# Performance work log

Measured on AMD Instinct MI355X. Metric: run time of the kernel, lower is better.

Reference implementation:

```python
import jax, jax.numpy as jnp
import numpy as np

EMBED_DIM = 584  # module-global, used as softmax scale base (C ** -0.5)


def setup_inputs() -> dict:
    key = jax.random.key(0)
    ks = jax.random.split(key, 7)
    B, T, C, H, D = 16, 1024, 584, 8, 73
    x = jax.random.normal(ks[0], (B, T, C), dtype=jnp.float32)
    memory = jax.random.normal(ks[1], (B, T, C), dtype=jnp.float32)
    s = 0.02
    Wq = jax.random.normal(ks[2], (H, C, D), dtype=jnp.float32) * s
    Wk = jax.random.normal(ks[3], (H, C, D), dtype=jnp.float32) * s
    Wv = jax.random.normal(ks[4], (H, C, D), dtype=jnp.float32) * s
    Wp = jax.random.normal(ks[5], (C, C), dtype=jnp.float32) * s
    bp = jnp.zeros((C,), dtype=jnp.float32)
    return {"x": x, "memory": memory, "Wq": Wq, "Wk": Wk, "Wv": Wv, "Wp": Wp, "bp": bp}


def reference(x, memory, Wq, Wk, Wv, Wp, bp):
    B, T, C = x.shape
    # per-head projections, vectorized over heads: [B, H, T, D]
    q = jnp.einsum('btc,hcd->bhtd', x, Wq)
    k = jnp.einsum('bsc,hcd->bhsd', memory, Wk)
    v = jnp.einsum('btc,hcd->bhtd', x, Wv)  # NOTE: value from x, per original code
    # scale uses full embed dim C (not head size), per original code
    scores = jnp.einsum('bhtd,bhsd->bhts', q, k) * (C ** -0.5)
    weights = jax.nn.softmax(scores, axis=-1)
    # dropout is identity in eval/reference mode
    out = jnp.einsum('bhts,bhsd->bhtd', weights, v)  # requires S == T (matches original)
    out = out.transpose(0, 2, 1, 3).reshape(B, T, C)  # concat heads on last dim
    out = out @ Wp + bp  # output projection (dropout identity)
    return out
```

## Files before the change

### kernel.cpp

```cpp
#include <hip/hip_runtime.h>
#include <hip/hip_bf16.h>

typedef unsigned short u16;
typedef __attribute__((ext_vector_type(4))) unsigned short u16x4;
typedef __attribute__((ext_vector_type(8))) unsigned short u16x8;
typedef __attribute__((ext_vector_type(8))) __bf16 bf16x8;
typedef __attribute__((ext_vector_type(4))) float f32x4;

#define BB 16
#define TSEQ 1024
#define CC 584
#define HH 8
#define DHD 73
#define NR (BB*TSEQ)
#define KPW 640
#define DP 96
#define HD (HH*DP)
#define NP3 768
#define PPITCH 88
#define CEXP 0.0596985934f

__device__ __forceinline__ u16 f2bf(float f) {
  __bf16 h = (__bf16)f;
  return __builtin_bit_cast(u16, h);
}
__device__ __forceinline__ bf16x8 as_bf(u16x8 v) { return __builtin_bit_cast(bf16x8, v); }

#define GLL16(g, l) __builtin_amdgcn_global_load_lds( \
    (const __attribute__((address_space(1))) void*)(g), \
    (__attribute__((address_space(3))) void*)(l), 16, 0, 0)

#define BARRIER() asm volatile("s_barrier" ::: "memory")
#define LGKM0()   asm volatile("s_waitcnt lgkmcnt(0)" ::: "memory")
#define VMW8()    asm volatile("s_waitcnt vmcnt(8)" ::: "memory")
#define VMW4()    asm volatile("s_waitcnt vmcnt(4)" ::: "memory")
#define VMW0()    asm volatile("s_waitcnt vmcnt(0)" ::: "memory")

#define PKA 10240
#define PKB2 720
#define PKC2 240
__global__ void pack_all_kernel(const float* __restrict__ x, const float* __restrict__ mem,
                                const float* __restrict__ Wq, const float* __restrict__ Wk,
                                const float* __restrict__ Wv, const float* __restrict__ Wp,
                                u16* __restrict__ xmb, u16* __restrict__ wt,
                                u16* __restrict__ wpt) {
  const int bidx = blockIdx.x;
  const int tid = threadIdx.x;
  if (bidx < PKA) {
    int idx = bidx * 256 + tid;
    int row = idx / (KPW / 8);
    int c8  = (idx % (KPW / 8)) * 8;
    u16x8 o = {0, 0, 0, 0, 0, 0, 0, 0};
    if (c8 < CC) {
      const float* src = (row < NR) ? &x[(size_t)row * CC + c8]
                                    : &mem[(size_t)(row - NR) * CC + c8];
      f32x4 a = *(const f32x4*)src;
      f32x4 b = *(const f32x4*)(src + 4);
#pragma unroll
      for (int t = 0; t < 4; t++) { o[t] = f2bf(a[t]); o[4 + t] = f2bf(b[t]); }
    }
    *(u16x8*)&xmb[(size_t)row * KPW + c8] = o;
  } else if (bidx < PKA + PKB2) {
    const int base = (bidx - PKA) * 2048 + tid;
#pragma unroll
    for (int e = 0; e < 8; e++) {
      int idx = base + e * 256;
      int w   = idx / (HD * KPW);
      int rem = idx % (HD * KPW);
      int n = rem / KPW;
      int k = rem % KPW;
      int h = n / DP, d = n % DP;
      u16 val = 0;
      if (d < DHD && k < CC) {
        const float* W = (w == 0) ? Wq : ((w == 1) ? Wv : Wk);
        val = f2bf(W[((size_t)h * CC + k) * DHD + d]);
      }
      wt[idx] = val;
    }
  } else {
    const int base = (bidx - PKA - PKB2) * 2048 + tid;
#pragma unroll
    for (int e = 0; e < 8; e++) {
      int idx = base + e * 256;
      int n = idx / KPW;
      int c = idx % KPW;
      u16 val = 0;
      if (n < CC && c < CC) val = f2bf(Wp[(size_t)c * CC + n]);
      wpt[idx] = val;
    }
  }
}


template <int BUF, int MH>
__device__ __forceinline__ void rd_a(bf16x8 (&a)[4][2], const u16* lds, int arow,
                                     int sw0, int sw1) {
#pragma unroll
  for (int mq = 0; mq < 4; mq++) {
    const int r = BUF * 32768 + MH * 8192 + arow + mq * 1024;
    a[mq][0] = as_bf(*(const u16x8*)&lds[r + sw0]);
    a[mq][1] = as_bf(*(const u16x8*)&lds[r + sw1]);
  }
}
template <int BUF, int NH>
__device__ __forceinline__ void rd_b(bf16x8 (&b)[2][2], const u16* lds, int brow,
                                     int sw0, int sw1) {
#pragma unroll
  for (int nq = 0; nq < 2; nq++) {
    const int r = BUF * 32768 + 16384 + NH * 8192 + brow + nq * 1024;
    b[nq][0] = as_bf(*(const u16x8*)&lds[r + sw0]);
    b[nq][1] = as_bf(*(const u16x8*)&lds[r + sw1]);
  }
}
template <int BUF, int RG>
__device__ __forceinline__ void stg(const u16* gA, const u16* gB, u16* ldst, int t) {
  const u16* src = (RG < 2) ? gA : gB;
  const int rrow = (RG & 1) * 128;
  const int loff = BUF * 32768 + (RG >> 1) * 16384 + (RG & 1) * 8192;
  GLL16(src + (size_t)rrow * KPW + (size_t)t * 64, ldst + loff);
  GLL16(src + (size_t)(rrow + 64) * KPW + (size_t)t * 64, ldst + loff + 4096);
}
template <int MH, int NH>
__device__ __forceinline__ void mmq(f32x4 (&acc)[8][4], const bf16x8 (&a)[4][2],
                                    const bf16x8 (&b)[2][2]) {
  __builtin_amdgcn_s_setprio(1);
#pragma unroll
  for (int mq = 0; mq < 4; mq++)
#pragma unroll
    for (int nq = 0; nq < 2; nq++) {
      f32x4 c = acc[MH * 4 + mq][NH * 2 + nq];
      c = __builtin_amdgcn_mfma_f32_16x16x32_bf16(a[mq][0], b[nq][0], c, 0, 0, 0);
      c = __builtin_amdgcn_mfma_f32_16x16x32_bf16(a[mq][1], b[nq][1], c, 0, 0, 0);
      acc[MH * 4 + mq][NH * 2 + nq] = c;
    }
  __builtin_amdgcn_s_setprio(0);
}

template <int MODE>
__global__ __launch_bounds__(512, 2) void gemm8_kernel(
    const u16* __restrict__ A, const u16* __restrict__ Bt,
    void* __restrict__ CoutV, void* __restrict__ CoutV2,
    const float* __restrict__ bias) {
  extern __shared__ u16 lds[];
  const int tid  = threadIdx.x;
  const int lane = tid & 63;
  const int q15  = lane & 15;
  const int quad = lane >> 4;
  const int wave = tid >> 6;
  const int wmi  = wave >> 2;
  const int wni  = wave & 3;

  const int cpx = gridDim.x >> 3;
  const int bid = (blockIdx.x & 7) * cpx + (blockIdx.x >> 3);

  int m0, n0, npart;
  if (MODE == 4) {
    if (bid < 384) {
      m0 = (bid / 6) * 256; int nt = bid % 6;
      n0 = nt * 256; npart = (nt >= 3) ? 1 : 0;
    } else {
      int b2 = bid - 384;
      m0 = NR + (b2 / 3) * 256; n0 = 1536 + (b2 % 3) * 256; npart = 2;
    }
  } else {
    m0 = (bid / 3) * 256; n0 = (bid % 3) * 256; npart = 0;
  }

  const int tr   = tid >> 3;
  const int scol = ((tid & 7) ^ (tr & 7)) * 8;
  const u16* gA = &A[(size_t)(m0 + tr) * KPW + scol];
  const u16* gB = &Bt[(size_t)(n0 + tr) * KPW + scol];
  u16* ldst = &lds[tid * 8];

  const int rb  = q15 & 7;
  const int sw0 = (quad ^ rb) * 8;
  const int sw1 = ((quad + 4) ^ rb) * 8;
  const int arow = (wmi * 64 + q15) * 64;
  const int brow = (wni * 32 + q15) * 64;

  f32x4 acc[8][4];
#pragma unroll
  for (int i = 0; i < 8; i++)
#pragma unroll
    for (int j = 0; j < 4; j++) acc[i][j] = (f32x4){0.f, 0.f, 0.f, 0.f};
  bf16x8 a[4][2], b0[2][2], b1[2][2];

  stg<0, 0>(gA, gB, ldst, 0);
  stg<0, 2>(gA, gB, ldst, 0);
  stg<0, 3>(gA, gB, ldst, 0);
  stg<0, 1>(gA, gB, ldst, 0);
  stg<1, 0>(gA, gB, ldst, 1);
  stg<1, 2>(gA, gB, ldst, 1);
  VMW8(); BARRIER();

#pragma unroll 1
  for (int i = 0; i < 5; ++i) {
    const int t1 = 2 * i + 1;
    const int t2 = 2 * i + 2;
    const int t3 = 2 * i + 3;
    const bool st = (i < 4);
    rd_a<0, 0>(a, lds, arow, sw0, sw1);
    rd_b<0, 0>(b0, lds, brow, sw0, sw1);
    stg<1, 3>(gA, gB, ldst, t1);
    stg<1, 1>(gA, gB, ldst, t1);
    VMW8(); BARRIER(); LGKM0();
    mmq<0, 0>(acc, a, b0);
    BARRIER();
    rd_b<0, 1>(b1, lds, brow, sw0, sw1);
    BARRIER(); LGKM0();
    mmq<0, 1>(acc, a, b1);
    BARRIER();
    rd_a<0, 1>(a, lds, arow, sw0, sw1);
    BARRIER(); LGKM0();
    mmq<1, 0>(acc, a, b0);
    BARRIER();
    if (st) { stg<0, 0>(gA, gB, ldst, t2); stg<0, 2>(gA, gB, ldst, t2); VMW8(); }
    else { VMW4(); }
    BARRIER();
    mmq<1, 1>(acc, a, b1);
    BARRIER();
    rd_a<1, 0>(a, lds, arow, sw0, sw1);
    rd_b<1, 0>(b0, lds, brow, sw0, sw1);
    if (st) { stg<0, 3>(gA, gB, ldst, t2); stg<0, 1>(gA, gB, ldst, t2); VMW8(); }
    else { VMW0(); }
    BARRIER(); LGKM0();
    mmq<0, 0>(acc, a, b0);
    BARRIER();
    rd_b<1, 1>(b1, lds, brow, sw0, sw1);
    BARRIER(); LGKM0();
    mmq<0, 1>(acc, a, b1);
    BARRIER();
    rd_a<1, 1>(a, lds, arow, sw0, sw1);
    BARRIER(); LGKM0();
    mmq<1, 0>(acc, a, b0);
    BARRIER();
    if (st) { stg<1, 0>(gA, gB, ldst, t3); stg<1, 2>(gA, gB, ldst, t3); VMW8(); }
    BARRIER();
    mmq<1, 1>(acc, a, b1);
    BARRIER();
  }

  const int rowb = m0 + wmi * 64 + quad * 4;
  const int colb = n0 + wni * 32 + q15;
#pragma unroll
  for (int mh = 0; mh < 2; mh++)
#pragma unroll
    for (int mq = 0; mq < 4; mq++)
#pragma unroll
      for (int nh = 0; nh < 2; nh++)
#pragma unroll
        for (int nq = 0; nq < 2; nq++) {
          const f32x4 av = acc[mh * 4 + mq][nh * 2 + nq];
          const int row = rowb + mh * 128 + mq * 16;
          const int col = colb + nh * 128 + nq * 16;
          if (MODE == 4) {
            if (npart == 2) {
              u16* Cout = (u16*)CoutV2;
              const int rk = row - NR;
              const int ck = col - 1536;
#pragma unroll
              for (int r = 0; r < 4; r++)
                Cout[(size_t)(rk + r) * HD + ck] = f2bf(av[r]);
            } else if (npart == 0) {
              u16* Cout = (u16*)CoutV;
#pragma unroll
              for (int r = 0; r < 4; r++)
                Cout[(size_t)(row + r) * HD + col] = f2bf(av[r]);
            } else {
              u16* Cout = (u16*)CoutV;
              const int vn = col - HD;
              const int bb = row >> 10;
              const int tl = row & 1023;
              u16x4 pk;
#pragma unroll
              for (int r = 0; r < 4; r++) pk[r] = f2bf(av[r]);
              *(u16x4*)&Cout[(size_t)(NR * HD) + ((size_t)(bb * HD + vn)) * TSEQ + tl] = pk;
            }
          } else {
            if (col < CC) {
              float* Cout = (float*)CoutV;
              const float bvv = bias[col];
#pragma unroll
              for (int r = 0; r < 4; r++)
                Cout[(size_t)(row + r) * CC + col] = av[r] + bvv;
            }
          }
        }
}

__global__ __launch_bounds__(256, 3) void attn_kernel(
    const u16* __restrict__ qb, const u16* __restrict__ kb,
    const u16* __restrict__ vt, u16* __restrict__ attn) {
  __shared__ u16 smem[128 * 96 + 64 * 104 + 96 * 72];
  u16* Qs = smem;
  u16* Ks = smem + 128 * 96;
  u16* Vs = smem + 128 * 96 + 64 * 104;
  u16* Pt = smem;

  const int tid  = threadIdx.x;
  const int lane = tid & 63;
  const int wave = tid >> 6;
  const int q15  = lane & 15;
  const int quad = lane >> 4;
  const int bid  = blockIdx.x;
  const int loc  = bid >> 3;
  const int pair = (bid & 7) * 16 + (loc >> 3);
  const int b  = pair >> 3;
  const int h  = pair & 7;
  const int t0 = (loc & 7) * 128;
  const int wq0 = wave * 32;

  int krow[3], kc[3], vrow[3], vc[3];
#pragma unroll
  for (int p = 0; p < 3; p++) {
    int qk = tid + 256 * p;
    krow[p] = qk / 12; kc[p] = (qk % 12) * 8;
    int qv = tid + 256 * p;
    vrow[p] = qv / 8;  vc[p] = (qv % 8) * 8;
  }
  const u16* kbase = &kb[(size_t)(b * TSEQ) * HD + h * DP];
  const u16* vbase = &vt[(size_t)(b * HD + h * DP) * TSEQ];

  for (int q = tid; q < 128 * 12; q += 256) {
    int row = q / 12, c8 = (q % 12) * 8;
    *(u16x8*)&Qs[row * 96 + c8] =
        *(const u16x8*)&qb[(size_t)(b * TSEQ + t0 + row) * HD + h * DP + c8];
  }
  if (tid < 128) {
    const u16x8 z = {0, 0, 0, 0, 0, 0, 0, 0};
    size_t base = (size_t)(b * TSEQ + t0 + tid) * KPW + CC;
#pragma unroll
    for (int c = 0; c < (KPW - CC) / 8; c++) *(u16x8*)&attn[base + c * 8] = z;
  }
  __syncthreads();

  bf16x8 aq[2][3];
#pragma unroll
  for (int n = 0; n < 2; n++)
#pragma unroll
    for (int kcx = 0; kcx < 3; kcx++)
      aq[n][kcx] = as_bf(*(const u16x8*)&Qs[(wq0 + n * 16 + q15) * 96 + kcx * 32 + quad * 8]);

  float lsum[2] = {0.f, 0.f};
  f32x4 oacc[2][6];
#pragma unroll
  for (int m = 0; m < 2; m++)
#pragma unroll
    for (int jd = 0; jd < 6; jd++) oacc[m][jd] = (f32x4){0.f, 0.f, 0.f, 0.f};

  u16* Ptw = &Pt[wave * 32 * PPITCH];

  u16x8 kreg[3], vreg[3];
#pragma unroll
  for (int p = 0; p < 3; p++) {
    kreg[p] = *(const u16x8*)&kbase[(size_t)krow[p] * HD + kc[p]];
    vreg[p] = *(const u16x8*)&vbase[(size_t)vrow[p] * TSEQ + vc[p]];
  }

  for (int si = 0; si < 16; ++si) {
#pragma unroll
    for (int p = 0; p < 3; p++) {
      *(u16x8*)&Ks[krow[p] * 104 + kc[p]] = kreg[p];
      *(u16x8*)&Vs[vrow[p] * 72 + vc[p]]  = vreg[p];
    }
    __syncthreads();

    if (si < 15) {
      const int s1 = (si + 1) * 64;
#pragma unroll
      for (int p = 0; p < 3; p++) {
        kreg[p] = *(const u16x8*)&kbase[(size_t)(s1 + krow[p]) * HD + kc[p]];
        vreg[p] = *(const u16x8*)&vbase[(size_t)vrow[p] * TSEQ + s1 + vc[p]];
      }
    }

    f32x4 st[4][2];
#pragma unroll
    for (int mt = 0; mt < 4; mt++)
#pragma unroll
      for (int n = 0; n < 2; n++) st[mt][n] = (f32x4){0.f, 0.f, 0.f, 0.f};
    __builtin_amdgcn_s_setprio(1);
#pragma unroll
    for (int kcx = 0; kcx < 3; kcx++) {
      bf16x8 ak[4];
#pragma unroll
      for (int mt = 0; mt < 4; mt++)
        ak[mt] = as_bf(*(const u16x8*)&Ks[(mt * 16 + q15) * 104 + kcx * 32 + quad * 8]);
#pragma unroll
      for (int mt = 0; mt < 4; mt++)
#pragma unroll
        for (int n = 0; n < 2; n++)
          st[mt][n] = __builtin_amdgcn_mfma_f32_16x16x32_bf16(ak[mt], aq[n][kcx], st[mt][n], 0, 0, 0);
    }
    __builtin_amdgcn_s_setprio(0);

#pragma unroll
    for (int mt = 0; mt < 4; mt++)
#pragma unroll
      for (int n = 0; n < 2; n++) {
        f32x4 pv;
#pragma unroll
        for (int r = 0; r < 4; r++) pv[r] = __builtin_amdgcn_exp2f(st[mt][n][r] * CEXP);
        lsum[n] += (pv[0] + pv[1]) + (pv[2] + pv[3]);
        u16x4 pk;
#pragma unroll
        for (int r = 0; r < 4; r++) pk[r] = f2bf(pv[r]);
        *(u16x4*)&Ptw[(n * 16 + q15) * PPITCH + mt * 16 + quad * 4] = pk;
      }

    __builtin_amdgcn_s_setprio(1);
#pragma unroll
    for (int kcx = 0; kcx < 2; kcx++) {
      bf16x8 ap[2];
#pragma unroll
      for (int m = 0; m < 2; m++)
        ap[m] = as_bf(*(const u16x8*)&Ptw[(m * 16 + q15) * PPITCH + kcx * 32 + quad * 8]);
#pragma unroll
      for (int jd = 0; jd < 6; jd++) {
        bf16x8 bv = as_bf(*(const u16x8*)&Vs[(jd * 16 + q15) * 72 + kcx * 32 + quad * 8]);
#pragma unroll
        for (int m = 0; m < 2; m++)
          oacc[m][jd] = __builtin_amdgcn_mfma_f32_16x16x32_bf16(ap[m], bv, oacc[m][jd], 0, 0, 0);
      }
    }
    __builtin_amdgcn_s_setprio(0);
    __syncthreads();
  }

  float lr[2];
#pragma unroll
  for (int n = 0; n < 2; n++) {
    float s = lsum[n];
    s += __shfl_xor(s, 16);
    s += __shfl_xor(s, 32);
    lr[n] = s;
  }

#pragma unroll
  for (int m = 0; m < 2; m++) {
#pragma unroll
    for (int r = 0; r < 4; r++) {
      const float inv = 1.f / __shfl(lr[m], quad * 4 + r);
      const int trow = t0 + wq0 + m * 16 + quad * 4 + r;
#pragma unroll
      for (int jd = 0; jd < 5; jd++) {
        const int d = jd * 16 + q15;
        if (d < DHD)
          attn[(size_t)(b * TSEQ + trow) * KPW + h * DHD + d] = f2bf(oacc[m][jd][r] * inv);
      }
    }
  }
}


extern "C" void kernel_launch(void* const* d_in, const int* in_sizes, int n_in,
                              void* d_out, int out_size, void* d_ws, size_t ws_size,
                              hipStream_t stream) {
  const float* x   = (const float*)d_in[0];
  const float* mem = (const float*)d_in[1];
  const float* Wq  = (const float*)d_in[2];
  const float* Wk  = (const float*)d_in[3];
  const float* Wv  = (const float*)d_in[4];
  const float* Wp  = (const float*)d_in[5];
  const float* bp  = (const float*)d_in[6];
  float* out = (float*)d_out;

  char* ws = (char*)d_ws;
  const size_t SZ_XMB = (size_t)2 * NR * KPW * 2;
  const size_t SZ_WT  = (size_t)3 * HD * KPW * 2;
  const size_t SZ_WPT = (size_t)NP3 * KPW * 2;
  const size_t SZ_QB  = (size_t)NR * HD * 2;

  u16* xmb    = (u16*)(ws);
  u16* attn_o = (u16*)(ws);
  u16* wt     = (u16*)(ws + SZ_XMB);
  u16* wp_t   = (u16*)(ws + SZ_XMB + SZ_WT);
  u16* q_buf  = (u16*)(ws + SZ_XMB + SZ_WT + SZ_WPT);
  u16* vt_buf = q_buf + (size_t)NR * HD;
  u16* k_buf  = (u16*)(ws + SZ_XMB + SZ_WT + SZ_WPT + 2 * SZ_QB);

  (void)in_sizes; (void)n_in; (void)out_size; (void)ws_size;

  static bool s_attr = false;
  if (!s_attr) {
    (void)hipFuncSetAttribute((const void*)gemm8_kernel<4>,
                              hipFuncAttributeMaxDynamicSharedMemorySize, 131072);
    (void)hipFuncSetAttribute((const void*)gemm8_kernel<2>,
                              hipFuncAttributeMaxDynamicSharedMemorySize, 131072);
    s_attr = true;
  }

  pack_all_kernel<<<PKA + PKB2 + PKC2, 256, 0, stream>>>(x, mem, Wq, Wk, Wv, Wp,
                                                         xmb, wt, wp_t);

  gemm8_kernel<4><<<576, 512, 131072, stream>>>(xmb, wt, q_buf, k_buf, nullptr);

  attn_kernel<<<BB * HH * (TSEQ / 128), 256, 0, stream>>>(q_buf, k_buf, vt_buf, attn_o);

  gemm8_kernel<2><<<192, 512, 131072, stream>>>(attn_o, wp_t, out, nullptr, bp);
}
```

Measured before the change: 301.9 us.

## Retile GEMM to 256x192 blocks with simpler double-buffered pipeline

The projection GEMMs move from 256x256 output tiles to 256x192. Each wave now covers 48 columns, and the LDS buffer shrinks to 114688 bytes. The main loop is rewritten as a per-K-tile double-buffered schedule with fewer barriers and no explicit lgkmcnt waits, and the grid grows to 768 and 256 blocks. This is meant to cut wasted padded columns (HD=768 and 584 padded to 768 divide evenly by 192) and improve load balance. The attention kernel also drops its s_setprio calls. Removing the lgkm waits relies on the compiler inserting them, and the new tiling lowers per-block operand reuse.

```diff
diff --git a/kernel.cpp b/kernel.cpp
--- a/kernel.cpp
+++ b/kernel.cpp
@@ -31,9 +31,8 @@
     (__attribute__((address_space(3))) void*)(l), 16, 0, 0)
 
 #define BARRIER() asm volatile("s_barrier" ::: "memory")
-#define LGKM0()   asm volatile("s_waitcnt lgkmcnt(0)" ::: "memory")
-#define VMW8()    asm volatile("s_waitcnt vmcnt(8)" ::: "memory")
-#define VMW4()    asm volatile("s_waitcnt vmcnt(4)" ::: "memory")
+#define VMW7()    asm volatile("s_waitcnt vmcnt(7)" ::: "memory")
+#define VMW2()    asm volatile("s_waitcnt vmcnt(2)" ::: "memory")
 #define VMW0()    asm volatile("s_waitcnt vmcnt(0)" ::: "memory")
 
 #define PKA 10240
@@ -92,46 +91,47 @@
 }
 
 
-template <int BUF, int MH>
-__device__ __forceinline__ void rd_a(bf16x8 (&a)[4][2], const u16* lds, int arow,
-                                     int sw0, int sw1) {
+__device__ __forceinline__ void rd_a3(bf16x8 (&a)[4][2], const u16* lds, int base,
+                                      int sw0, int sw1) {
 #pragma unroll
   for (int mq = 0; mq < 4; mq++) {
-    const int r = BUF * 32768 + MH * 8192 + arow + mq * 1024;
+    const int r = base + mq * 1024;
     a[mq][0] = as_bf(*(const u16x8*)&lds[r + sw0]);
     a[mq][1] = as_bf(*(const u16x8*)&lds[r + sw1]);
   }
 }
-template <int BUF, int NH>
-__device__ __forceinline__ void rd_b(bf16x8 (&b)[2][2], const u16* lds, int brow,
-                                     int sw0, int sw1) {
-#pragma unroll
-  for (int nq = 0; nq < 2; nq++) {
-    const int r = BUF * 32768 + 16384 + NH * 8192 + brow + nq * 1024;
+__device__ __forceinline__ void rd_b3(bf16x8 (&b)[3][2], const u16* lds, int base,
+                                      int sw0, int sw1) {
+#pragma unroll
+  for (int nq = 0; nq < 3; nq++) {
+    const int r = base + nq * 1024;
     b[nq][0] = as_bf(*(const u16x8*)&lds[r + sw0]);
     b[nq][1] = as_bf(*(const u16x8*)&lds[r + sw1]);
   }
 }
-template <int BUF, int RG>
-__device__ __forceinline__ void stg(const u16* gA, const u16* gB, u16* ldst, int t) {
-  const u16* src = (RG < 2) ? gA : gB;
-  const int rrow = (RG & 1) * 128;
-  const int loff = BUF * 32768 + (RG >> 1) * 16384 + (RG & 1) * 8192;
-  GLL16(src + (size_t)rrow * KPW + (size_t)t * 64, ldst + loff);
-  GLL16(src + (size_t)(rrow + 64) * KPW + (size_t)t * 64, ldst + loff + 4096);
-}
-template <int MH, int NH>
-__device__ __forceinline__ void mmq(f32x4 (&acc)[8][4], const bf16x8 (&a)[4][2],
-                                    const bf16x8 (&b)[2][2]) {
+__device__ __forceinline__ void s_a1(const u16* gA, u16* ldst, int t, int lb) {
+  GLL16(gA + (size_t)128 * KPW + (size_t)t * 64, ldst + lb + 8192);
+  GLL16(gA + (size_t)192 * KPW + (size_t)t * 64, ldst + lb + 12288);
+}
+__device__ __forceinline__ void s_a0b(const u16* gA, const u16* gB, u16* ldst,
+                                      int t, int lb) {
+  GLL16(gA + (size_t)t * 64, ldst + lb);
+  GLL16(gA + (size_t)64 * KPW + (size_t)t * 64, ldst + lb + 4096);
+  GLL16(gB + (size_t)t * 64, ldst + lb + 16384);
+  GLL16(gB + (size_t)64 * KPW + (size_t)t * 64, ldst + lb + 20480);
+  GLL16(gB + (size_t)128 * KPW + (size_t)t * 64, ldst + lb + 24576);
+}
+__device__ __forceinline__ void mm43(f32x4 (&acc)[4][3], const bf16x8 (&a)[4][2],
+                                     const bf16x8 (&b)[3][2]) {
   __builtin_amdgcn_s_setprio(1);
 #pragma unroll
   for (int mq = 0; mq < 4; mq++)
 #pragma unroll
-    for (int nq = 0; nq < 2; nq++) {
-      f32x4 c = acc[MH * 4 + mq][NH * 2 + nq];
+    for (int nq = 0; nq < 3; nq++) {
+      f32x4 c = acc[mq][nq];
       c = __builtin_amdgcn_mfma_f32_16x16x32_bf16(a[mq][0], b[nq][0], c, 0, 0, 0);
       c = __builtin_amdgcn_mfma_f32_16x16x32_bf16(a[mq][1], b[nq][1], c, 0, 0, 0);
-      acc[MH * 4 + mq][NH * 2 + nq] = c;
+      acc[mq][nq] = c;
     }
   __builtin_amdgcn_s_setprio(0);
 }
@@ -155,15 +155,15 @@
 
   int m0, n0, npart;
   if (MODE == 4) {
-    if (bid < 384) {
-      m0 = (bid / 6) * 256; int nt = bid % 6;
-      n0 = nt * 256; npart = (nt >= 3) ? 1 : 0;
+    if (bid < 512) {
+      m0 = (bid >> 3) * 256; int nt = bid & 7;
+      n0 = nt * 192; npart = (nt >= 4) ? 1 : 0;
     } else {
-      int b2 = bid - 384;
-      m0 = NR + (b2 / 3) * 256; n0 = 1536 + (b2 % 3) * 256; npart = 2;
+      int b2 = bid - 512;
+      m0 = NR + (b2 >> 2) * 256; n0 = 1536 + (b2 & 3) * 192; npart = 2;
     }
   } else {
-    m0 = (bid / 3) * 256; n0 = (bid % 3) * 256; npart = 0;
+    m0 = (bid >> 2) * 256; n0 = (bid & 3) * 192; npart = 0;
   }
 
   const int tr   = tid >> 3;
@@ -176,116 +176,85 @@
   const int sw0 = (quad ^ rb) * 8;
   const int sw1 = ((quad + 4) ^ rb) * 8;
   const int arow = (wmi * 64 + q15) * 64;
-  const int brow = (wni * 32 + q15) * 64;
-
-  f32x4 acc[8][4];
-#pragma unroll
-  for (int i = 0; i < 8; i++)
-#pragma unroll
-    for (int j = 0; j < 4; j++) acc[i][j] = (f32x4){0.f, 0.f, 0.f, 0.f};
-  bf16x8 a[4][2], b0[2][2], b1[2][2];
-
-  stg<0, 0>(gA, gB, ldst, 0);
-  stg<0, 2>(gA, gB, ldst, 0);
-  stg<0, 3>(gA, gB, ldst, 0);
-  stg<0, 1>(gA, gB, ldst, 0);
-  stg<1, 0>(gA, gB, ldst, 1);
-  stg<1, 2>(gA, gB, ldst, 1);
-  VMW8(); BARRIER();
+  const int brow = (wni * 48 + q15) * 64;
+
+  f32x4 acc[2][4][3];
+#pragma unroll
+  for (int i = 0; i < 2; i++)
+#pragma unroll
+    for (int j = 0; j < 4; j++)
+#pragma unroll
+      for (int k = 0; k < 3; k++) acc[i][j][k] = (f32x4){0.f, 0.f, 0.f, 0.f};
+  bf16x8 a[4][2], b[3][2];
+
+  s_a0b(gA, gB, ldst, 0, 0);
+  s_a1(gA, ldst, 0, 0);
+  s_a0b(gA, gB, ldst, 1, 28672);
+  VMW7(); BARRIER();
 
 #pragma unroll 1
-  for (int i = 0; i < 5; ++i) {
-    const int t1 = 2 * i + 1;
-    const int t2 = 2 * i + 2;
-    const int t3 = 2 * i + 3;
-    const bool st = (i < 4);
-    rd_a<0, 0>(a, lds, arow, sw0, sw1);
-    rd_b<0, 0>(b0, lds, brow, sw0, sw1);
-    stg<1, 3>(gA, gB, ldst, t1);
-    stg<1, 1>(gA, gB, ldst, t1);
-    VMW8(); BARRIER(); LGKM0();
-    mmq<0, 0>(acc, a, b0);
+  for (int t = 0; t < 10; ++t) {
+    const int lb = (t & 1) * 28672;
+    const int lbo = lb ^ 28672;
+    rd_a3(a, lds, lb + arow, sw0, sw1);
+    rd_b3(b, lds, lb + 16384 + brow, sw0, sw1);
+    if (t < 9) s_a1(gA, ldst, t + 1, lbo);
+    if (t == 9) { VMW0(); } else { VMW7(); }
     BARRIER();
-    rd_b<0, 1>(b1, lds, brow, sw0, sw1);
-    BARRIER(); LGKM0();
-    mmq<0, 1>(acc, a, b1);
+    mm43(acc[0], a, b);
     BARRIER();
-    rd_a<0, 1>(a, lds, arow, sw0, sw1);
-    BARRIER(); LGKM0();
-    mmq<1, 0>(acc, a, b0);
+    rd_a3(a, lds, lb + 8192 + arow, sw0, sw1);
+    if (t < 8) { s_a0b(gA, gB, ldst, t + 2, lb); VMW7(); }
+    else if (t == 8) { VMW2(); }
     BARRIER();
-    if (st) { stg<0, 0>(gA, gB, ldst, t2); stg<0, 2>(gA, gB, ldst, t2); VMW8(); }
-    else { VMW4(); }
+    mm43(acc[1], a, b);
     BARRIER();
-    mmq<1, 1>(acc, a, b1);
-    BARRIER();
-    rd_a<1, 0>(a, lds, arow, sw0, sw1);
-    rd_b<1, 0>(b0, lds, brow, sw0, sw1);
-    if (st) { stg<0, 3>(gA, gB, ldst, t2); stg<0, 1>(gA, gB, ldst, t2); VMW8(); }
-    else { VMW0(); }
-    BARRIER(); LGKM0();
-    mmq<0, 0>(acc, a, b0);
-    BARRIER();
-    rd_b<1, 1>(b1, lds, brow, sw0, sw1);
-    BARRIER(); LGKM0();
-    mmq<0, 1>(acc, a, b1);
-    BARRIER();
-    rd_a<1, 1>(a, lds, arow, sw0, sw1);
-    BARRIER(); LGKM0();
-    mmq<1, 0>(acc, a, b0);
-    BARRIER();
-    if (st) { stg<1, 0>(gA, gB, ldst, t3); stg<1, 2>(gA, gB, ldst, t3); VMW8(); }
-    BARRIER();
-    mmq<1, 1>(acc, a, b1);
-    BARRIER();
   }
 
   const int rowb = m0 + wmi * 64 + quad * 4;
-  const int colb = n0 + wni * 32 + q15;
+  const int colb = n0 + wni * 48 + q15;
 #pragma unroll
   for (int mh = 0; mh < 2; mh++)
 #pragma unroll
     for (int mq = 0; mq < 4; mq++)
 #pragma unroll
-      for (int nh = 0; nh < 2; nh++)
-#pragma unroll
-        for (int nq = 0; nq < 2; nq++) {
-          const f32x4 av = acc[mh * 4 + mq][nh * 2 + nq];
-          const int row = rowb + mh * 128 + mq * 16;
-          const int col = colb + nh * 128 + nq * 16;
-          if (MODE == 4) {
-            if (npart == 2) {
-              u16* Cout = (u16*)CoutV2;
-              const int rk = row - NR;
-              const int ck = col - 1536;
-#pragma unroll
-              for (int r = 0; r < 4; r++)
-                Cout[(size_t)(rk + r) * HD + ck] = f2bf(av[r]);
-            } else if (npart == 0) {
-              u16* Cout = (u16*)CoutV;
-#pragma unroll
-              for (int r = 0; r < 4; r++)
-                Cout[(size_t)(row + r) * HD + col] = f2bf(av[r]);
-            } else {
-              u16* Cout = (u16*)CoutV;
-              const int vn = col - HD;
-              const int bb = row >> 10;
-              const int tl = row & 1023;
-              u16x4 pk;
-#pragma unroll
-              for (int r = 0; r < 4; r++) pk[r] = f2bf(av[r]);
-              *(u16x4*)&Cout[(size_t)(NR * HD) + ((size_t)(bb * HD + vn)) * TSEQ + tl] = pk;
-            }
+      for (int nq = 0; nq < 3; nq++) {
+        const f32x4 av = acc[mh][mq][nq];
+        const int row = rowb + mh * 128 + mq * 16;
+        const int col = colb + nq * 16;
+        if (MODE == 4) {
+          if (npart == 2) {
+            u16* Cout = (u16*)CoutV2;
+            const int rk = row - NR;
+            const int ck = col - 1536;
+#pragma unroll
+            for (int r = 0; r < 4; r++)
+              Cout[(size_t)(rk + r) * HD + ck] = f2bf(av[r]);
+          } else if (npart == 0) {
+            u16* Cout = (u16*)CoutV;
+#pragma unroll
+            for (int r = 0; r < 4; r++)
+              Cout[(size_t)(row + r) * HD + col] = f2bf(av[r]);
           } else {
-            if (col < CC) {
-              float* Cout = (float*)CoutV;
-              const float bvv = bias[col];
-#pragma unroll
-              for (int r = 0; r < 4; r++)
-                Cout[(size_t)(row + r) * CC + col] = av[r] + bvv;
-            }
+            u16* Cout = (u16*)CoutV;
+            const int vn = col - HD;
+            const int bb = row >> 10;
+            const int tl = row & 1023;
+            u16x4 pk;
+#pragma unroll
+            for (int r = 0; r < 4; r++) pk[r] = f2bf(av[r]);
+            *(u16x4*)&Cout[(size_t)(NR * HD) + ((size_t)(bb * HD + vn)) * TSEQ + tl] = pk;
+          }
+        } else {
+          if (col < CC) {
+            float* Cout = (float*)CoutV;
+            const float bvv = bias[col];
+#pragma unroll
+            for (int r = 0; r < 4; r++)
+              Cout[(size_t)(row + r) * CC + col] = av[r] + bvv;
           }
         }
+      }
 }
 
 __global__ __launch_bounds__(256, 3) void attn_kernel(
@@ -379,7 +348,6 @@
     for (int mt = 0; mt < 4; mt++)
 #pragma unroll
       for (int n = 0; n < 2; n++) st[mt][n] = (f32x4){0.f, 0.f, 0.f, 0.f};
-    __builtin_amdgcn_s_setprio(1);
 #pragma unroll
     for (int kcx = 0; kcx < 3; kcx++) {
       bf16x8 ak[4];
@@ -392,7 +360,6 @@
         for (int n = 0; n < 2; n++)
           st[mt][n] = __builtin_amdgcn_mfma_f32_16x16x32_bf16(ak[mt], aq[n][kcx], st[mt][n], 0, 0, 0);
     }
-    __builtin_amdgcn_s_setprio(0);
 
 #pragma unroll
     for (int mt = 0; mt < 4; mt++)
@@ -408,7 +375,6 @@
         *(u16x4*)&Ptw[(n * 16 + q15) * PPITCH + mt * 16 + quad * 4] = pk;
       }
 
-    __builtin_amdgcn_s_setprio(1);
 #pragma unroll
     for (int kcx = 0; kcx < 2; kcx++) {
       bf16x8 ap[2];
@@ -423,7 +389,6 @@
           oacc[m][jd] = __builtin_amdgcn_mfma_f32_16x16x32_bf16(ap[m], bv, oacc[m][jd], 0, 0, 0);
       }
     }
-    __builtin_amdgcn_s_setprio(0);
     __syncthreads();
   }
 
@@ -484,18 +449,18 @@
   static bool s_attr = false;
   if (!s_attr) {
     (void)hipFuncSetAttribute((const void*)gemm8_kernel<4>,
-                              hipFuncAttributeMaxDynamicSharedMemorySize, 131072);
+                              hipFuncAttributeMaxDynamicSharedMemorySize, 114688);
     (void)hipFuncSetAttribute((const void*)gemm8_kernel<2>,
-                              hipFuncAttributeMaxDynamicSharedMemorySize, 131072);
+                              hipFuncAttributeMaxDynamicSharedMemorySize, 114688);
     s_attr = true;
   }
 
   pack_all_kernel<<<PKA + PKB2 + PKC2, 256, 0, stream>>>(x, mem, Wq, Wk, Wv, Wp,
                                                          xmb, wt, wp_t);
 
-  gemm8_kernel<4><<<576, 512, 131072, stream>>>(xmb, wt, q_buf, k_buf, nullptr);
+  gemm8_kernel<4><<<768, 512, 114688, stream>>>(xmb, wt, q_buf, k_buf, nullptr);
 
   attn_kernel<<<BB * HH * (TSEQ / 128), 256, 0, stream>>>(q_buf, k_buf, vt_buf, attn_o);
 
-  gemm8_kernel<2><<<192, 512, 131072, stream>>>(attn_o, wp_t, out, nullptr, bp);
-}
+  gemm8_kernel<2><<<256, 512, 114688, stream>>>(attn_o, wp_t, out, nullptr, bp);
+}
```

New measurement: 289.3 us. -4.2%, faster.
